# Kernel optimization log

Measured on AMD Instinct MI355X. Metric: run time of the kernel, lower is better.

The kernel has to match this reference:

```python
import jax, jax.numpy as jnp
import numpy as np

N = 50000        # nodes
E = 800000       # edges (avg degree 16)
IN = 256         # in_feature
HID = 32         # hidden per head
HEADS = 4        # gat_heads
OUT = 64         # out_feature
SLOPE = 0.2      # PyG GATConv default negative_slope


def _gat_layer(x, src, dst, edge_weight, W, a_src, a_dst, b, heads, ch, concat):
    """One GATConv: linear -> per-edge attention logits -> segment softmax over
    incoming edges of each dst node -> weighted scatter-sum. edge_weight scales
    the unnormalized attention (log-space edge weighting, identity at init=1)."""
    n = x.shape[0]
    h = (x @ W).reshape(n, heads, ch)                       # [N,H,C]
    al_s = jnp.einsum('nhc,hc->nh', h, a_src)               # [N,H]
    al_d = jnp.einsum('nhc,hc->nh', h, a_dst)               # [N,H]
    logit = jax.nn.leaky_relu(al_s[src] + al_d[dst], SLOPE) # [E,H]
    m = jax.lax.stop_gradient(jax.ops.segment_max(logit, dst, num_segments=n))
    e = jnp.exp(logit - m[dst]) * edge_weight[:, None]      # [E,H]
    denom = jax.ops.segment_sum(e, dst, num_segments=n)     # [N,H]
    alpha = e / (denom[dst] + 1e-16)                        # [E,H]
    out = jax.ops.segment_sum(h[src] * alpha[..., None], dst, num_segments=n)
    out = out.reshape(n, heads * ch) if concat else out.mean(axis=1)
    return out + b


def setup_inputs() -> dict:
    key = jax.random.key(0)
    ks = jax.random.split(key, 14)
    s = 0.1
    x = jax.random.normal(ks[0], (N, IN), jnp.float32)
    edge_index = jax.random.randint(ks[1], (2, E), 0, N, dtype=jnp.int64)
    edge_weight = jnp.ones((E,), jnp.float32)
    D1 = HEADS * HID
    W1 = jax.random.normal(ks[2], (IN, D1), jnp.float32) * s
    a_src1 = jax.random.normal(ks[3], (HEADS, HID), jnp.float32) * s
    a_dst1 = jax.random.normal(ks[4], (HEADS, HID), jnp.float32) * s
    b1 = jnp.zeros((D1,), jnp.float32)
    W2 = jax.random.normal(ks[5], (D1, D1), jnp.float32) * s
    a_src2 = jax.random.normal(ks[6], (HEADS, HID), jnp.float32) * s
    a_dst2 = jax.random.normal(ks[7], (HEADS, HID), jnp.float32) * s
    b2 = jnp.zeros((D1,), jnp.float32)
    W3 = jax.random.normal(ks[8], (D1, OUT), jnp.float32) * s
    a_src3 = jax.random.normal(ks[9], (1, OUT), jnp.float32) * s
    a_dst3 = jax.random.normal(ks[10], (1, OUT), jnp.float32) * s
    b3 = jnp.zeros((OUT,), jnp.float32)
    return dict(x=x, edge_index=edge_index, edge_weight=edge_weight,
                W1=W1, a_src1=a_src1, a_dst1=a_dst1, b1=b1,
                W2=W2, a_src2=a_src2, a_dst2=a_dst2, b2=b2,
                W3=W3, a_src3=a_src3, a_dst3=a_dst3, b3=b3)


def reference(x, edge_index, edge_weight,
              W1, a_src1, a_dst1, b1,
              W2, a_src2, a_dst2, b2,
              W3, a_src3, a_dst3, b3):
    src, dst = edge_index[0], edge_index[1]
    h = _gat_layer(x, src, dst, edge_weight, W1, a_src1, a_dst1, b1, HEADS, HID, True)
    h = jax.nn.relu(h)  # dropout = identity in eval mode
    h = _gat_layer(h, src, dst, edge_weight, W2, a_src2, a_dst2, b2, HEADS, HID, True)
    h = jax.nn.relu(h)
    out = _gat_layer(h, src, dst, edge_weight, W3, a_src3, a_dst3, b3, 1, OUT, False)
    return out
```

## Files before the change

### kernel.cpp

```cpp
#include <hip/hip_runtime.h>
#include <math.h>

#define NNODES 50000
#define NEDGES 800000

#define BIN_SHIFT 9
#define BIN_W 512
#define NBINS 98
#define CAP 12288
#define ATILE 4096
#define NBINBLK ((NEDGES + ATILE - 1) / ATILE)

typedef _Float16 f16;
typedef __attribute__((ext_vector_type(2))) _Float16 f16x2;
typedef __attribute__((ext_vector_type(4))) _Float16 f16x4;
typedef __attribute__((ext_vector_type(8))) _Float16 f16x8;
typedef __attribute__((ext_vector_type(4))) float f32x4;

__device__ __forceinline__ float leaky02(float v) { return v > 0.f ? v : 0.2f * v; }

__device__ __forceinline__ void wave_lds_fence() {
  __asm__ volatile("s_waitcnt lgkmcnt(0)" ::: "memory");
}


__global__ __launch_bounds__(256) void init_kernel(int* __restrict__ binCursor,
                                                   const float* __restrict__ W1,
                                                   const float* __restrict__ W2,
                                                   const float* __restrict__ W3,
                                                   f16* __restrict__ WT1,
                                                   f16* __restrict__ WT2,
                                                   f16* __restrict__ WT3) {
  int gid = blockIdx.x * 256 + threadIdx.x;
  int stride = gridDim.x * 256;
  if (gid < NBINS) binCursor[gid] = 0;
  for (int i = gid; i < 32768; i += stride) {
    int d = i >> 8, k = i & 255;
    WT1[i] = (f16)W1[k * 128 + d];
  }
  for (int i = gid; i < 16384; i += stride) {
    int d = i >> 7, k = i & 127;
    WT2[i] = (f16)W2[k * 128 + d];
  }
  for (int i = gid; i < 8192; i += stride) {
    int d = i >> 7, k = i & 127;
    WT3[i] = (f16)W3[k * 64 + d];
  }
}


__device__ __forceinline__ void bin_body(int bid,
                                         const int* __restrict__ dst,
                                         const int* __restrict__ src,
                                         const float* __restrict__ ew,
                                         int* __restrict__ binCursor,
                                         int2* __restrict__ binned, int ne) {
  __shared__ int cnt[NBINS];
  __shared__ int gbase[NBINS];
  int tid = threadIdx.x;
  int t0 = bid * ATILE;
  if (tid < NBINS) cnt[tid] = 0;
  __syncthreads();
  int saved[ATILE / 256];
  #pragma unroll
  for (int u = 0; u < ATILE / 256; ++u) {
    int i = t0 + u * 256 + tid;
    int v = 0;
    if (i < ne) {
      int d = dst[i];
      int idx = atomicAdd(&cnt[d >> BIN_SHIFT], 1);
      v = d | (idx << 16);
    }
    saved[u] = v;
  }
  __syncthreads();
  if (tid < NBINS) gbase[tid] = atomicAdd(&binCursor[tid], cnt[tid]);
  __syncthreads();
  #pragma unroll
  for (int u = 0; u < ATILE / 256; ++u) {
    int i = t0 + u * 256 + tid;
    if (i < ne) {
      int v = saved[u];
      int d = v & 0xffff;
      int idx = (int)((unsigned)v >> 16);
      int b = d >> BIN_SHIFT;
      int slot = gbase[b] + idx;
      if (slot < CAP)
        binned[(size_t)b * CAP + slot] =
            make_int2(src[i] | (d << 16), __float_as_int(ew[i]));
    }
  }
}


__global__ __launch_bounds__(256) void build_kernel(const int2* __restrict__ binned,
                                                    const int* __restrict__ binCursor,
                                                    int* __restrict__ offsets,
                                                    int2* __restrict__ edgeSW, int n) {
  __shared__ int sizes[NBINS];
  __shared__ int cnt[BIN_W];
  __shared__ int wsum[4];
  __shared__ int bstartS;
  int tid = threadIdx.x;
  int b = blockIdx.x;
  if (tid < NBINS) sizes[tid] = binCursor[tid];
  cnt[tid] = 0;
  cnt[tid + 256] = 0;
  __syncthreads();
  if (tid == 0) {
    int s = 0;
    for (int k = 0; k < b; ++k) s += (sizes[k] < CAP ? sizes[k] : CAP);
    bstartS = s;
  }
  int mySize = sizes[b];
  if (mySize > CAP) mySize = CAP;
  __syncthreads();
  const int2* mybin = binned + (size_t)b * CAP;
  for (int i = tid; i < mySize; i += 256)
    atomicAdd(&cnt[((unsigned)mybin[i].x >> 16) - b * BIN_W], 1);
  __syncthreads();
  int c0 = cnt[2 * tid], c1 = cnt[2 * tid + 1];
  int s2 = c0 + c1;
  int lane = tid & 63, wid = tid >> 6;
  int incl = s2;
  #pragma unroll
  for (int o = 1; o < 64; o <<= 1) {
    int u = __shfl_up(incl, o, 64);
    if (lane >= o) incl += u;
  }
  if (lane == 63) wsum[wid] = incl;
  __syncthreads();
  if (tid == 0) {
    int r = 0;
    #pragma unroll
    for (int w = 0; w < 4; ++w) { int t = wsum[w]; wsum[w] = r; r += t; }
  }
  __syncthreads();
  int excl0 = bstartS + wsum[wid] + incl - s2;
  int excl1 = excl0 + c0;
  int node0 = b * BIN_W;
  if (node0 + 2 * tid < n)     offsets[node0 + 2 * tid]     = excl0;
  if (node0 + 2 * tid + 1 < n) offsets[node0 + 2 * tid + 1] = excl1;
  if (b == NBINS - 1 && tid == 0) offsets[n] = bstartS + mySize;
  __syncthreads();
  cnt[2 * tid] = excl0;
  cnt[2 * tid + 1] = excl1;
  __syncthreads();
  for (int i = tid; i < mySize; i += 256) {
    int2 r = mybin[i];
    int dloc = (int)((unsigned)r.x >> 16) - b * BIN_W;
    int pos = atomicAdd(&cnt[dloc], 1);
    edgeSW[pos] = make_int2(r.x & 0xffff, r.y);
  }
}


template<typename AT, int BN, int H>
__device__ __forceinline__ void gemm_body(int bid,
                                          const AT* __restrict__ A,
                                          const f16* __restrict__ BT,
                                          f16* __restrict__ C,
                                          const float* __restrict__ a_src,
                                          const float* __restrict__ a_dst,
                                          float* __restrict__ als,
                                          float* __restrict__ ald,
                                          int M, int K) {
  constexpr int BM = 64;
  constexpr int WN = BN / 2;
  constexpr int MT = 2, NT = WN / 16;
  __shared__ f16 As[BM * 72];
  __shared__ f16 Bs[BN * 72];
  __shared__ float redS[2][2][32], redD[2][2][32];
  int tid = threadIdx.x;
  int lane = tid & 63, wave = tid >> 6;
  int wm = wave & 1, wn = wave >> 1;
  int row0 = bid * BM;
  int quad = lane >> 4, cc = lane & 15;

  f32x4 acc[MT][NT];
  #pragma unroll
  for (int mt = 0; mt < MT; ++mt)
    #pragma unroll
    for (int nt = 0; nt < NT; ++nt)
      acc[mt][nt] = (f32x4){0.f, 0.f, 0.f, 0.f};

  for (int k0 = 0; k0 < K; k0 += 64) {
    __syncthreads();
    if constexpr (sizeof(AT) == 4) {
      #pragma unroll
      for (int i = 0; i < 4; ++i) {
        int r = i * 16 + (tid >> 4);
        int kc = (tid & 15) * 4;
        float4 av = make_float4(0.f, 0.f, 0.f, 0.f);
        if (row0 + r < M) av = *(const float4*)&A[(size_t)(row0 + r) * K + k0 + kc];
        *(f16x4*)&As[r * 72 + kc] = (f16x4){(f16)av.x, (f16)av.y, (f16)av.z, (f16)av.w};
      }
    } else {
      #pragma unroll
      for (int i = 0; i < 2; ++i) {
        int r = i * 32 + (tid >> 3);
        int kc = (tid & 7) * 8;
        f16x8 hv = {0, 0, 0, 0, 0, 0, 0, 0};
        if (row0 + r < M) hv = *(const f16x8*)&A[(size_t)(row0 + r) * K + k0 + kc];
        *(f16x8*)&As[r * 72 + kc] = hv;
      }
    }
    #pragma unroll
    for (int i = 0; i < BN / 32; ++i) {
      int d = i * 32 + (tid >> 3);
      int kc = (tid & 7) * 8;
      *(f16x8*)&Bs[d * 72 + kc] = *(const f16x8*)&BT[(size_t)d * K + k0 + kc];
    }
    __syncthreads();
    #pragma unroll
    for (int ki = 0; ki < 2; ++ki) {
      f16x8 a[MT], b[NT];
      #pragma unroll
      for (int mt = 0; mt < MT; ++mt)
        a[mt] = *(const f16x8*)&As[(wm * 32 + mt * 16 + cc) * 72 + ki * 32 + quad * 8];
      #pragma unroll
      for (int nt = 0; nt < NT; ++nt)
        b[nt] = *(const f16x8*)&Bs[(wn * WN + nt * 16 + cc) * 72 + ki * 32 + quad * 8];
      #pragma unroll
      for (int mt = 0; mt < MT; ++mt)
        #pragma unroll
        for (int nt = 0; nt < NT; ++nt)
          acc[mt][nt] = __builtin_amdgcn_mfma_f32_16x16x32_f16(a[mt], b[nt], acc[mt][nt], 0, 0, 0);
    }
  }

  float asv[NT], adv[NT];
  #pragma unroll
  for (int nt = 0; nt < NT; ++nt) {
    int ch = wn * WN + nt * 16 + cc;
    asv[nt] = a_src[ch];
    adv[nt] = a_dst[ch];
  }

  #pragma unroll
  for (int mt = 0; mt < MT; ++mt)
    #pragma unroll
    for (int v = 0; v < 4; ++v) {
      int row = row0 + wm * 32 + mt * 16 + quad * 4 + v;
      if (row < M) {
        #pragma unroll
        for (int nt = 0; nt < NT; ++nt)
          C[(size_t)row * BN + wn * WN + nt * 16 + cc] = (f16)acc[mt][nt][v];
      }
      if constexpr (H == 4) {
        float s0 = acc[mt][0][v] * asv[0] + acc[mt][1][v] * asv[1];
        float s1 = acc[mt][2][v] * asv[2] + acc[mt][3][v] * asv[3];
        float d0 = acc[mt][0][v] * adv[0] + acc[mt][1][v] * adv[1];
        float d1 = acc[mt][2][v] * adv[2] + acc[mt][3][v] * adv[3];
        #pragma unroll
        for (int o = 1; o < 16; o <<= 1) {
          s0 += __shfl_xor(s0, o);
          s1 += __shfl_xor(s1, o);
          d0 += __shfl_xor(d0, o);
          d1 += __shfl_xor(d1, o);
        }
        if (cc == 0 && row < M) {
          *(float2*)&als[row * 4 + 2 * wn] = make_float2(s0, s1);
          *(float2*)&ald[row * 4 + 2 * wn] = make_float2(d0, d1);
        }
      } else {
        float s0 = acc[mt][0][v] * asv[0] + acc[mt][1][v] * asv[1];
        float d0 = acc[mt][0][v] * adv[0] + acc[mt][1][v] * adv[1];
        #pragma unroll
        for (int o = 1; o < 16; o <<= 1) {
          s0 += __shfl_xor(s0, o);
          d0 += __shfl_xor(d0, o);
        }
        int r = mt * 16 + quad * 4 + v;
        if (cc == 0) { redS[wm][wn][r] = s0; redD[wm][wn][r] = d0; }
      }
    }
  if constexpr (H == 1) {
    __syncthreads();
    #pragma unroll
    for (int mt = 0; mt < MT; ++mt)
      #pragma unroll
      for (int v = 0; v < 4; ++v) {
        int row = row0 + wm * 32 + mt * 16 + quad * 4 + v;
        int r = mt * 16 + quad * 4 + v;
        if (wn == 0 && cc == 0 && row < M) {
          als[row] = redS[wm][0][r] + redS[wm][1][r];
          ald[row] = redD[wm][0][r] + redD[wm][1][r];
        }
      }
  }
}

template<typename AT, int BN, int H>
__global__ __launch_bounds__(256) void gemm_mfma_kernel(const AT* __restrict__ A,
                                                        const f16* __restrict__ BT,
                                                        f16* __restrict__ C,
                                                        const float* __restrict__ a_src,
                                                        const float* __restrict__ a_dst,
                                                        float* __restrict__ als,
                                                        float* __restrict__ ald,
                                                        int M, int K) {
  gemm_body<AT, BN, H>(blockIdx.x, A, BT, C, a_src, a_dst, als, ald, M, K);
}


__global__ __launch_bounds__(256) void fused_front_kernel(const int* __restrict__ dst,
                                                          const int* __restrict__ src,
                                                          const float* __restrict__ ew,
                                                          int* __restrict__ binCursor,
                                                          int2* __restrict__ binned, int ne,
                                                          const float* __restrict__ A,
                                                          const f16* __restrict__ BT,
                                                          f16* __restrict__ C,
                                                          const float* __restrict__ a_src,
                                                          const float* __restrict__ a_dst,
                                                          float* __restrict__ als,
                                                          float* __restrict__ ald,
                                                          int M, int K) {
  if (blockIdx.x < NBINBLK)
    bin_body(blockIdx.x, dst, src, ew, binCursor, binned, ne);
  else
    gemm_body<float, 128, 4>(blockIdx.x - NBINBLK, A, BT, C, a_src, a_dst, als, ald, M, K);
}


template<bool RELU>
__global__ __launch_bounds__(256) void aggregate4_kernel(const f16* __restrict__ h16,
                                                         const float* __restrict__ als,
                                                         const float* __restrict__ ald,
                                                         const int* __restrict__ offsets,
                                                         const int2* __restrict__ edgeSW,
                                                         const float* __restrict__ bias,
                                                         f16* __restrict__ out, int n_nodes) {
  __shared__ int   swS[8][32];
  __shared__ float swW[8][4][36];
  int hw = threadIdx.x >> 5;
  int hl = threadIdx.x & 31;
  int node = blockIdx.x * 8 + hw;
  bool valid = node < n_nodes;
  int nodeC = valid ? node : n_nodes - 1;
  int start = offsets[nodeC], end = offsets[nodeC + 1];
  int deg = valid ? end - start : 0;

  float4 aldv = *(const float4*)&ald[nodeC * 4];

  int s0 = 0; float wgt0 = 0.f;
  float v0 = 0.f, v1 = 0.f, v2 = 0.f, v3 = 0.f;
  float m0 = -INFINITY, m1 = -INFINITY, m2 = -INFINITY, m3 = -INFINITY;
  if (hl < deg) {
    int2 e = edgeSW[start + hl];
    s0 = e.x;
    wgt0 = __int_as_float(e.y);
    float4 a4 = *(const float4*)&als[s0 * 4];
    v0 = leaky02(a4.x + aldv.x); m0 = v0;
    v1 = leaky02(a4.y + aldv.y); m1 = v1;
    v2 = leaky02(a4.z + aldv.z); m2 = v2;
    v3 = leaky02(a4.w + aldv.w); m3 = v3;
  }
  for (int j = start + 32 + hl; j < end; j += 32) {
    int2 e = edgeSW[j];
    float4 a4 = *(const float4*)&als[e.x * 4];
    m0 = fmaxf(m0, leaky02(a4.x + aldv.x));
    m1 = fmaxf(m1, leaky02(a4.y + aldv.y));
    m2 = fmaxf(m2, leaky02(a4.z + aldv.z));
    m3 = fmaxf(m3, leaky02(a4.w + aldv.w));
  }
  #pragma unroll
  for (int o = 16; o > 0; o >>= 1) {
    m0 = fmaxf(m0, __shfl_xor(m0, o, 32));
    m1 = fmaxf(m1, __shfl_xor(m1, o, 32));
    m2 = fmaxf(m2, __shfl_xor(m2, o, 32));
    m3 = fmaxf(m3, __shfl_xor(m3, o, 32));
  }
  float w0 = 0.f, w1 = 0.f, w2 = 0.f, w3 = 0.f;
  if (hl < deg) {
    w0 = __expf(v0 - m0) * wgt0;
    w1 = __expf(v1 - m1) * wgt0;
    w2 = __expf(v2 - m2) * wgt0;
    w3 = __expf(v3 - m3) * wgt0;
  }
  swS[hw][hl] = s0;
  swW[hw][0][hl] = w0;
  swW[hw][1][hl] = w1;
  swW[hw][2][hl] = w2;
  swW[hw][3][hl] = w3;
  wave_lds_fence();

  int h2 = hl >> 4, l16 = hl & 15;
  int head = l16 >> 2;
  float acc0 = 0.f, acc1 = 0.f, acc2 = 0.f, acc3 = 0.f;
  float acc4 = 0.f, acc5 = 0.f, acc6 = 0.f, acc7 = 0.f;
  float dd = 0.f;
  int cn = deg < 32 ? deg : 32;
  int nb = (cn + 15) >> 4;
  for (int b = 0; b < nb; ++b) {
    int j0 = b * 16 + h2 * 8;
    int4   sa = *(const int4*)&swS[hw][j0];
    int4   sb = *(const int4*)&swS[hw][j0 + 4];
    float4 wa = *(const float4*)&swW[hw][head][j0];
    float4 wb = *(const float4*)&swW[hw][head][j0 + 4];
    int   sj[8] = {sa.x, sa.y, sa.z, sa.w, sb.x, sb.y, sb.z, sb.w};
    float wj[8] = {wa.x, wa.y, wa.z, wa.w, wb.x, wb.y, wb.z, wb.w};
    f16x8 hv[8];
    #pragma unroll
    for (int u = 0; u < 8; ++u)
      hv[u] = *(const f16x8*)&h16[(size_t)sj[u] * 128 + 8 * l16];
    #pragma unroll
    for (int u = 0; u < 8; ++u) {
      dd += wj[u];
      acc0 += wj[u] * (float)hv[u][0];
      acc1 += wj[u] * (float)hv[u][1];
      acc2 += wj[u] * (float)hv[u][2];
      acc3 += wj[u] * (float)hv[u][3];
      acc4 += wj[u] * (float)hv[u][4];
      acc5 += wj[u] * (float)hv[u][5];
      acc6 += wj[u] * (float)hv[u][6];
      acc7 += wj[u] * (float)hv[u][7];
    }
  }
  for (int base = start + 32; base < end; base += 32) {
    int cnt = end - base; if (cnt > 32) cnt = 32;
    int st = 0; float u0 = 0.f, u1 = 0.f, u2 = 0.f, u3 = 0.f;
    if (hl < cnt) {
      int2 e = edgeSW[base + hl];
      st = e.x;
      float wg = __int_as_float(e.y);
      float4 a4 = *(const float4*)&als[st * 4];
      u0 = __expf(leaky02(a4.x + aldv.x) - m0) * wg;
      u1 = __expf(leaky02(a4.y + aldv.y) - m1) * wg;
      u2 = __expf(leaky02(a4.z + aldv.z) - m2) * wg;
      u3 = __expf(leaky02(a4.w + aldv.w) - m3) * wg;
    }
    for (int jj = h2; jj < cnt; jj += 2) {
      int sjr = __shfl(st, jj, 32);
      float t0 = __shfl(u0, jj, 32), t1 = __shfl(u1, jj, 32);
      float t2 = __shfl(u2, jj, 32), t3 = __shfl(u3, jj, 32);
      float wr = head == 0 ? t0 : head == 1 ? t1 : head == 2 ? t2 : t3;
      f16x8 hv = *(const f16x8*)&h16[(size_t)sjr * 128 + 8 * l16];
      dd += wr;
      acc0 += wr * (float)hv[0];
      acc1 += wr * (float)hv[1];
      acc2 += wr * (float)hv[2];
      acc3 += wr * (float)hv[3];
      acc4 += wr * (float)hv[4];
      acc5 += wr * (float)hv[5];
      acc6 += wr * (float)hv[6];
      acc7 += wr * (float)hv[7];
    }
  }

  acc0 += __shfl_xor(acc0, 16, 32);
  acc1 += __shfl_xor(acc1, 16, 32);
  acc2 += __shfl_xor(acc2, 16, 32);
  acc3 += __shfl_xor(acc3, 16, 32);
  acc4 += __shfl_xor(acc4, 16, 32);
  acc5 += __shfl_xor(acc5, 16, 32);
  acc6 += __shfl_xor(acc6, 16, 32);
  acc7 += __shfl_xor(acc7, 16, 32);
  dd   += __shfl_xor(dd, 16, 32);

  if (valid && h2 == 0) {
    float inv = 1.f / (dd + 1e-16f);
    float4 bv0 = *(const float4*)&bias[8 * l16];
    float4 bv1 = *(const float4*)&bias[8 * l16 + 4];
    float o0 = acc0 * inv + bv0.x, o1 = acc1 * inv + bv0.y;
    float o2 = acc2 * inv + bv0.z, o3 = acc3 * inv + bv0.w;
    float o4 = acc4 * inv + bv1.x, o5 = acc5 * inv + bv1.y;
    float o6 = acc6 * inv + bv1.z, o7 = acc7 * inv + bv1.w;
    if (RELU) {
      o0 = fmaxf(o0, 0.f); o1 = fmaxf(o1, 0.f);
      o2 = fmaxf(o2, 0.f); o3 = fmaxf(o3, 0.f);
      o4 = fmaxf(o4, 0.f); o5 = fmaxf(o5, 0.f);
      o6 = fmaxf(o6, 0.f); o7 = fmaxf(o7, 0.f);
    }
    *(f16x8*)&out[(size_t)node * 128 + 8 * l16] =
        (f16x8){(f16)o0, (f16)o1, (f16)o2, (f16)o3, (f16)o4, (f16)o5, (f16)o6, (f16)o7};
  }
}

__global__ __launch_bounds__(256) void aggregate1_kernel(const f16* __restrict__ h16,
                                                         const float* __restrict__ als,
                                                         const float* __restrict__ ald,
                                                         const int* __restrict__ offsets,
                                                         const int2* __restrict__ edgeSW,
                                                         const float* __restrict__ bias,
                                                         float* __restrict__ out, int n_nodes) {
  __shared__ int   s1s[8][32];
  __shared__ float w1s[8][32];
  int hw = threadIdx.x >> 5;
  int hl = threadIdx.x & 31;
  int node = blockIdx.x * 8 + hw;
  bool valid = node < n_nodes;
  int nodeC = valid ? node : n_nodes - 1;
  int start = offsets[nodeC], end = offsets[nodeC + 1];
  int deg = valid ? end - start : 0;

  float ald0 = ald[nodeC];
  int s0 = 0; float wgt0 = 0.f, v0 = 0.f, m0 = -INFINITY;
  if (hl < deg) {
    int2 e = edgeSW[start + hl];
    s0 = e.x;
    wgt0 = __int_as_float(e.y);
    v0 = leaky02(als[s0] + ald0);
    m0 = v0;
  }
  for (int j = start + 32 + hl; j < end; j += 32) {
    int2 e = edgeSW[j];
    m0 = fmaxf(m0, leaky02(als[e.x] + ald0));
  }
  #pragma unroll
  for (int o = 16; o > 0; o >>= 1) m0 = fmaxf(m0, __shfl_xor(m0, o, 32));

  float w0 = (hl < deg) ? __expf(v0 - m0) * wgt0 : 0.f;
  s1s[hw][hl] = s0;
  w1s[hw][hl] = w0;
  wave_lds_fence();

  int h2 = hl >> 4, l16 = hl & 15;
  float aX = 0.f, aY = 0.f, aZ = 0.f, aW = 0.f, dd = 0.f;
  int cn = deg < 32 ? deg : 32;
  int nb = (cn + 15) >> 4;
  for (int b = 0; b < nb; ++b) {
    int j0 = b * 16 + h2 * 8;
    int4   sa = *(const int4*)&s1s[hw][j0];
    int4   sb = *(const int4*)&s1s[hw][j0 + 4];
    float4 wa = *(const float4*)&w1s[hw][j0];
    float4 wb = *(const float4*)&w1s[hw][j0 + 4];
    int   sj[8] = {sa.x, sa.y, sa.z, sa.w, sb.x, sb.y, sb.z, sb.w};
    float wj[8] = {wa.x, wa.y, wa.z, wa.w, wb.x, wb.y, wb.z, wb.w};
    f16x4 hv[8];
    #pragma unroll
    for (int u = 0; u < 8; ++u)
      hv[u] = *(const f16x4*)&h16[(size_t)sj[u] * 64 + 4 * l16];
    #pragma unroll
    for (int u = 0; u < 8; ++u) {
      dd += wj[u];
      aX += wj[u] * (float)hv[u][0];
      aY += wj[u] * (float)hv[u][1];
      aZ += wj[u] * (float)hv[u][2];
      aW += wj[u] * (float)hv[u][3];
    }
  }
  for (int base = start + 32; base < end; base += 32) {
    int cnt = end - base; if (cnt > 32) cnt = 32;
    int st = 0; float u0 = 0.f;
    if (hl < cnt) {
      int2 e = edgeSW[base + hl];
      st = e.x;
      u0 = __expf(leaky02(als[st] + ald0) - m0) * __int_as_float(e.y);
    }
    for (int jj = h2; jj < cnt; jj += 2) {
      int sjr = __shfl(st, jj, 32);
      float wr = __shfl(u0, jj, 32);
      f16x4 hv = *(const f16x4*)&h16[(size_t)sjr * 64 + 4 * l16];
      dd += wr;
      aX += wr * (float)hv[0];
      aY += wr * (float)hv[1];
      aZ += wr * (float)hv[2];
      aW += wr * (float)hv[3];
    }
  }

  aX += __shfl_xor(aX, 16, 32);
  aY += __shfl_xor(aY, 16, 32);
  aZ += __shfl_xor(aZ, 16, 32);
  aW += __shfl_xor(aW, 16, 32);
  dd += __shfl_xor(dd, 16, 32);

  if (valid && h2 == 0) {
    float inv = 1.f / (dd + 1e-16f);
    float4 bv = *(const float4*)&bias[4 * l16];
    float4 ov = make_float4(aX * inv + bv.x, aY * inv + bv.y,
                            aZ * inv + bv.z, aW * inv + bv.w);
    *(float4*)&out[(size_t)node * 64 + 4 * l16] = ov;
  }
}


extern "C" void kernel_launch(void* const* d_in, const int* in_sizes, int n_in,
                              void* d_out, int out_size, void* d_ws, size_t ws_size,
                              hipStream_t stream) {
  const int N = NNODES, E = NEDGES;
  const float* x   = (const float*)d_in[0];
  const int*   ei  = (const int*)d_in[1];
  const float* ew  = (const float*)d_in[2];
  const float* W1  = (const float*)d_in[3];
  const float* as1 = (const float*)d_in[4];
  const float* ad1 = (const float*)d_in[5];
  const float* b1  = (const float*)d_in[6];
  const float* W2  = (const float*)d_in[7];
  const float* as2 = (const float*)d_in[8];
  const float* ad2 = (const float*)d_in[9];
  const float* b2  = (const float*)d_in[10];
  const float* W3  = (const float*)d_in[11];
  const float* as3 = (const float*)d_in[12];
  const float* ad3 = (const float*)d_in[13];
  const float* b3  = (const float*)d_in[14];
  const int* src = ei;
  const int* dst = ei + E;

  uint8_t* p = (uint8_t*)d_ws;
  auto carve = [&](size_t bytes) {
    void* r = (void*)p;
    p += (bytes + 255) & ~(size_t)255;
    return r;
  };
  int*   binCursor = (int*)carve((size_t)NBINS * 4);
  int*   offsets   = (int*)carve((size_t)(N + 1) * 4);
  int2*  binned    = (int2*)carve((size_t)NBINS * CAP * 8);
  int2*  edgeSW    = (int2*)carve((size_t)E * 8);
  float* als1      = (float*)carve((size_t)N * 4 * 4);
  float* ald1      = (float*)carve((size_t)N * 4 * 4);
  float* als2      = (float*)carve((size_t)N * 4 * 4);
  float* ald2      = (float*)carve((size_t)N * 4 * 4);
  float* als3      = (float*)carve((size_t)N * 4);
  float* ald3      = (float*)carve((size_t)N * 4);
  f16*   hA16      = (f16*)carve((size_t)N * 128 * 2);
  f16*   hB16      = (f16*)carve((size_t)N * 128 * 2);
  f16*   hC16      = (f16*)carve((size_t)N * 64 * 2);
  f16*   WT1       = (f16*)carve((size_t)256 * 128 * 2);
  f16*   WT2       = (f16*)carve((size_t)128 * 128 * 2);
  f16*   WT3       = (f16*)carve((size_t)128 * 64 * 2);

  int gemmGrid = (N + 63) / 64;
  int aggGrid = (N + 7) / 8;

  init_kernel<<<128, 256, 0, stream>>>(binCursor, W1, W2, W3, WT1, WT2, WT3);

  fused_front_kernel<<<NBINBLK + gemmGrid, 256, 0, stream>>>(
      dst, src, ew, binCursor, binned, E,
      x, WT1, hA16, as1, ad1, als1, ald1, N, 256);
  build_kernel<<<NBINS, 256, 0, stream>>>(binned, binCursor, offsets, edgeSW, N);

  aggregate4_kernel<true><<<aggGrid, 256, 0, stream>>>(hA16, als1, ald1, offsets, edgeSW,
                                                       b1, hB16, N);
  gemm_mfma_kernel<f16, 128, 4><<<gemmGrid, 256, 0, stream>>>(hB16, WT2, hA16, as2, ad2,
                                                              als2, ald2, N, 128);
  aggregate4_kernel<true><<<aggGrid, 256, 0, stream>>>(hA16, als2, ald2, offsets, edgeSW,
                                                       b2, hB16, N);
  gemm_mfma_kernel<f16, 64, 1><<<gemmGrid, 256, 0, stream>>>(hB16, WT3, hC16, as3, ad3,
                                                             als3, ald3, N, 128);
  aggregate1_kernel<<<aggGrid, 256, 0, stream>>>(hC16, als3, ald3, offsets, edgeSW,
                                                 b3, (float*)d_out, N);
}
```

Measured before the change: 270.8 us.

## Fuse layer aggregation with next-layer GEMM via shared-memory A tile

Layer-1 and layer-2 aggregation are merged with the following GEMM into one 512-thread kernel. Each block aggregates 64 nodes, writes the ReLU'd fp16 features straight into an LDS A-tile, then runs MFMA against the next weight matrix and computes the attention logits. This removes two kernel launches and the global write and re-read of the intermediate hidden features. In exchange, LDS use per block grows and the gather phase and the GEMM phase are serialized inside each block, which may lower occupancy and overlap.

```diff
diff --git a/kernel.cpp b/kernel.cpp
--- a/kernel.cpp
+++ b/kernel.cpp
@@ -170,7 +170,6 @@
   constexpr int MT = 2, NT = WN / 16;
   __shared__ f16 As[BM * 72];
   __shared__ f16 Bs[BN * 72];
-  __shared__ float redS[2][2][32], redD[2][2][32];
   int tid = threadIdx.x;
   int lane = tid & 63, wave = tid >> 6;
   int wm = wave & 1, wn = wave >> 1;
@@ -247,60 +246,22 @@
         for (int nt = 0; nt < NT; ++nt)
           C[(size_t)row * BN + wn * WN + nt * 16 + cc] = (f16)acc[mt][nt][v];
       }
-      if constexpr (H == 4) {
-        float s0 = acc[mt][0][v] * asv[0] + acc[mt][1][v] * asv[1];
-        float s1 = acc[mt][2][v] * asv[2] + acc[mt][3][v] * asv[3];
-        float d0 = acc[mt][0][v] * adv[0] + acc[mt][1][v] * adv[1];
-        float d1 = acc[mt][2][v] * adv[2] + acc[mt][3][v] * adv[3];
-        #pragma unroll
-        for (int o = 1; o < 16; o <<= 1) {
-          s0 += __shfl_xor(s0, o);
-          s1 += __shfl_xor(s1, o);
-          d0 += __shfl_xor(d0, o);
-          d1 += __shfl_xor(d1, o);
-        }
-        if (cc == 0 && row < M) {
-          *(float2*)&als[row * 4 + 2 * wn] = make_float2(s0, s1);
-          *(float2*)&ald[row * 4 + 2 * wn] = make_float2(d0, d1);
-        }
-      } else {
-        float s0 = acc[mt][0][v] * asv[0] + acc[mt][1][v] * asv[1];
-        float d0 = acc[mt][0][v] * adv[0] + acc[mt][1][v] * adv[1];
-        #pragma unroll
-        for (int o = 1; o < 16; o <<= 1) {
-          s0 += __shfl_xor(s0, o);
-          d0 += __shfl_xor(d0, o);
-        }
-        int r = mt * 16 + quad * 4 + v;
-        if (cc == 0) { redS[wm][wn][r] = s0; redD[wm][wn][r] = d0; }
-      }
-    }
-  if constexpr (H == 1) {
-    __syncthreads();
-    #pragma unroll
-    for (int mt = 0; mt < MT; ++mt)
-      #pragma unroll
-      for (int v = 0; v < 4; ++v) {
-        int row = row0 + wm * 32 + mt * 16 + quad * 4 + v;
-        int r = mt * 16 + quad * 4 + v;
-        if (wn == 0 && cc == 0 && row < M) {
-          als[row] = redS[wm][0][r] + redS[wm][1][r];
-          ald[row] = redD[wm][0][r] + redD[wm][1][r];
-        }
-      }
-  }
-}
-
-template<typename AT, int BN, int H>
-__global__ __launch_bounds__(256) void gemm_mfma_kernel(const AT* __restrict__ A,
-                                                        const f16* __restrict__ BT,
-                                                        f16* __restrict__ C,
-                                                        const float* __restrict__ a_src,
-                                                        const float* __restrict__ a_dst,
-                                                        float* __restrict__ als,
-                                                        float* __restrict__ ald,
-                                                        int M, int K) {
-  gemm_body<AT, BN, H>(blockIdx.x, A, BT, C, a_src, a_dst, als, ald, M, K);
+      float s0 = acc[mt][0][v] * asv[0] + acc[mt][1][v] * asv[1];
+      float s1 = acc[mt][2][v] * asv[2] + acc[mt][3][v] * asv[3];
+      float d0 = acc[mt][0][v] * adv[0] + acc[mt][1][v] * adv[1];
+      float d1 = acc[mt][2][v] * adv[2] + acc[mt][3][v] * adv[3];
+      #pragma unroll
+      for (int o = 1; o < 16; o <<= 1) {
+        s0 += __shfl_xor(s0, o);
+        s1 += __shfl_xor(s1, o);
+        d0 += __shfl_xor(d0, o);
+        d1 += __shfl_xor(d1, o);
+      }
+      if (cc == 0 && row < M) {
+        *(float2*)&als[row * 4 + 2 * wn] = make_float2(s0, s1);
+        *(float2*)&ald[row * 4 + 2 * wn] = make_float2(d0, d1);
+      }
+    }
 }
 
 
@@ -324,157 +285,267 @@
 }
 
 
-template<bool RELU>
-__global__ __launch_bounds__(256) void aggregate4_kernel(const f16* __restrict__ h16,
-                                                         const float* __restrict__ als,
-                                                         const float* __restrict__ ald,
-                                                         const int* __restrict__ offsets,
-                                                         const int2* __restrict__ edgeSW,
-                                                         const float* __restrict__ bias,
-                                                         f16* __restrict__ out, int n_nodes) {
-  __shared__ int   swS[8][32];
-  __shared__ float swW[8][4][36];
-  int hw = threadIdx.x >> 5;
-  int hl = threadIdx.x & 31;
-  int node = blockIdx.x * 8 + hw;
-  bool valid = node < n_nodes;
-  int nodeC = valid ? node : n_nodes - 1;
-  int start = offsets[nodeC], end = offsets[nodeC + 1];
-  int deg = valid ? end - start : 0;
-
-  float4 aldv = *(const float4*)&ald[nodeC * 4];
-
-  int s0 = 0; float wgt0 = 0.f;
-  float v0 = 0.f, v1 = 0.f, v2 = 0.f, v3 = 0.f;
-  float m0 = -INFINITY, m1 = -INFINITY, m2 = -INFINITY, m3 = -INFINITY;
-  if (hl < deg) {
-    int2 e = edgeSW[start + hl];
-    s0 = e.x;
-    wgt0 = __int_as_float(e.y);
-    float4 a4 = *(const float4*)&als[s0 * 4];
-    v0 = leaky02(a4.x + aldv.x); m0 = v0;
-    v1 = leaky02(a4.y + aldv.y); m1 = v1;
-    v2 = leaky02(a4.z + aldv.z); m2 = v2;
-    v3 = leaky02(a4.w + aldv.w); m3 = v3;
-  }
-  for (int j = start + 32 + hl; j < end; j += 32) {
-    int2 e = edgeSW[j];
-    float4 a4 = *(const float4*)&als[e.x * 4];
-    m0 = fmaxf(m0, leaky02(a4.x + aldv.x));
-    m1 = fmaxf(m1, leaky02(a4.y + aldv.y));
-    m2 = fmaxf(m2, leaky02(a4.z + aldv.z));
-    m3 = fmaxf(m3, leaky02(a4.w + aldv.w));
-  }
-  #pragma unroll
-  for (int o = 16; o > 0; o >>= 1) {
-    m0 = fmaxf(m0, __shfl_xor(m0, o, 32));
-    m1 = fmaxf(m1, __shfl_xor(m1, o, 32));
-    m2 = fmaxf(m2, __shfl_xor(m2, o, 32));
-    m3 = fmaxf(m3, __shfl_xor(m3, o, 32));
-  }
-  float w0 = 0.f, w1 = 0.f, w2 = 0.f, w3 = 0.f;
-  if (hl < deg) {
-    w0 = __expf(v0 - m0) * wgt0;
-    w1 = __expf(v1 - m1) * wgt0;
-    w2 = __expf(v2 - m2) * wgt0;
-    w3 = __expf(v3 - m3) * wgt0;
-  }
-  swS[hw][hl] = s0;
-  swW[hw][0][hl] = w0;
-  swW[hw][1][hl] = w1;
-  swW[hw][2][hl] = w2;
-  swW[hw][3][hl] = w3;
-  wave_lds_fence();
-
+template<int BN, int H>
+__global__ __launch_bounds__(512) void fused_aggemm_kernel(
+    const f16* __restrict__ hg,
+    const float* __restrict__ als_i,
+    const float* __restrict__ ald_i,
+    const int* __restrict__ offsets,
+    const int2* __restrict__ edgeSW,
+    const float* __restrict__ bias,
+    const f16* __restrict__ BT,
+    f16* __restrict__ C,
+    const float* __restrict__ a_src,
+    const float* __restrict__ a_dst,
+    float* __restrict__ als_o,
+    float* __restrict__ ald_o,
+    int n_nodes) {
+  constexpr int K = 128;
+  constexpr int BM = 64;
+  constexpr int WN = BN / 4;
+  constexpr int MT = 2, NT = WN / 16;
+  __shared__ f16 As[BM * 136];
+  __shared__ f16 Bs[BN * 72];
+  __shared__ int   swS[16][32];
+  __shared__ float swW[16][4][36];
+  __shared__ float redS[2][4][32], redD[2][4][32];
+
+  int tid = threadIdx.x;
+  int hw = tid >> 5, hl = tid & 31;
+  int row0 = blockIdx.x * BM;
   int h2 = hl >> 4, l16 = hl & 15;
   int head = l16 >> 2;
-  float acc0 = 0.f, acc1 = 0.f, acc2 = 0.f, acc3 = 0.f;
-  float acc4 = 0.f, acc5 = 0.f, acc6 = 0.f, acc7 = 0.f;
-  float dd = 0.f;
-  int cn = deg < 32 ? deg : 32;
-  int nb = (cn + 15) >> 4;
-  for (int b = 0; b < nb; ++b) {
-    int j0 = b * 16 + h2 * 8;
-    int4   sa = *(const int4*)&swS[hw][j0];
-    int4   sb = *(const int4*)&swS[hw][j0 + 4];
-    float4 wa = *(const float4*)&swW[hw][head][j0];
-    float4 wb = *(const float4*)&swW[hw][head][j0 + 4];
-    int   sj[8] = {sa.x, sa.y, sa.z, sa.w, sb.x, sb.y, sb.z, sb.w};
-    float wj[8] = {wa.x, wa.y, wa.z, wa.w, wb.x, wb.y, wb.z, wb.w};
-    f16x8 hv[8];
-    #pragma unroll
-    for (int u = 0; u < 8; ++u)
-      hv[u] = *(const f16x8*)&h16[(size_t)sj[u] * 128 + 8 * l16];
-    #pragma unroll
-    for (int u = 0; u < 8; ++u) {
-      dd += wj[u];
-      acc0 += wj[u] * (float)hv[u][0];
-      acc1 += wj[u] * (float)hv[u][1];
-      acc2 += wj[u] * (float)hv[u][2];
-      acc3 += wj[u] * (float)hv[u][3];
-      acc4 += wj[u] * (float)hv[u][4];
-      acc5 += wj[u] * (float)hv[u][5];
-      acc6 += wj[u] * (float)hv[u][6];
-      acc7 += wj[u] * (float)hv[u][7];
-    }
-  }
-  for (int base = start + 32; base < end; base += 32) {
-    int cnt = end - base; if (cnt > 32) cnt = 32;
-    int st = 0; float u0 = 0.f, u1 = 0.f, u2 = 0.f, u3 = 0.f;
-    if (hl < cnt) {
-      int2 e = edgeSW[base + hl];
-      st = e.x;
-      float wg = __int_as_float(e.y);
-      float4 a4 = *(const float4*)&als[st * 4];
-      u0 = __expf(leaky02(a4.x + aldv.x) - m0) * wg;
-      u1 = __expf(leaky02(a4.y + aldv.y) - m1) * wg;
-      u2 = __expf(leaky02(a4.z + aldv.z) - m2) * wg;
-      u3 = __expf(leaky02(a4.w + aldv.w) - m3) * wg;
-    }
-    for (int jj = h2; jj < cnt; jj += 2) {
-      int sjr = __shfl(st, jj, 32);
-      float t0 = __shfl(u0, jj, 32), t1 = __shfl(u1, jj, 32);
-      float t2 = __shfl(u2, jj, 32), t3 = __shfl(u3, jj, 32);
-      float wr = head == 0 ? t0 : head == 1 ? t1 : head == 2 ? t2 : t3;
-      f16x8 hv = *(const f16x8*)&h16[(size_t)sjr * 128 + 8 * l16];
-      dd += wr;
-      acc0 += wr * (float)hv[0];
-      acc1 += wr * (float)hv[1];
-      acc2 += wr * (float)hv[2];
-      acc3 += wr * (float)hv[3];
-      acc4 += wr * (float)hv[4];
-      acc5 += wr * (float)hv[5];
-      acc6 += wr * (float)hv[6];
-      acc7 += wr * (float)hv[7];
-    }
-  }
-
-  acc0 += __shfl_xor(acc0, 16, 32);
-  acc1 += __shfl_xor(acc1, 16, 32);
-  acc2 += __shfl_xor(acc2, 16, 32);
-  acc3 += __shfl_xor(acc3, 16, 32);
-  acc4 += __shfl_xor(acc4, 16, 32);
-  acc5 += __shfl_xor(acc5, 16, 32);
-  acc6 += __shfl_xor(acc6, 16, 32);
-  acc7 += __shfl_xor(acc7, 16, 32);
-  dd   += __shfl_xor(dd, 16, 32);
-
-  if (valid && h2 == 0) {
-    float inv = 1.f / (dd + 1e-16f);
-    float4 bv0 = *(const float4*)&bias[8 * l16];
-    float4 bv1 = *(const float4*)&bias[8 * l16 + 4];
-    float o0 = acc0 * inv + bv0.x, o1 = acc1 * inv + bv0.y;
-    float o2 = acc2 * inv + bv0.z, o3 = acc3 * inv + bv0.w;
-    float o4 = acc4 * inv + bv1.x, o5 = acc5 * inv + bv1.y;
-    float o6 = acc6 * inv + bv1.z, o7 = acc7 * inv + bv1.w;
-    if (RELU) {
-      o0 = fmaxf(o0, 0.f); o1 = fmaxf(o1, 0.f);
-      o2 = fmaxf(o2, 0.f); o3 = fmaxf(o3, 0.f);
-      o4 = fmaxf(o4, 0.f); o5 = fmaxf(o5, 0.f);
-      o6 = fmaxf(o6, 0.f); o7 = fmaxf(o7, 0.f);
-    }
-    *(f16x8*)&out[(size_t)node * 128 + 8 * l16] =
-        (f16x8){(f16)o0, (f16)o1, (f16)o2, (f16)o3, (f16)o4, (f16)o5, (f16)o6, (f16)o7};
+
+  for (int p = 0; p < 4; ++p) {
+    int node = row0 + p * 16 + hw;
+    bool valid = node < n_nodes;
+    int nodeC = valid ? node : n_nodes - 1;
+    int start = offsets[nodeC], end = offsets[nodeC + 1];
+    int deg = valid ? end - start : 0;
+
+    float4 aldv = *(const float4*)&ald_i[nodeC * 4];
+
+    int s0 = 0; float wgt0 = 0.f;
+    float v0 = 0.f, v1 = 0.f, v2 = 0.f, v3 = 0.f;
+    float m0 = -INFINITY, m1 = -INFINITY, m2 = -INFINITY, m3 = -INFINITY;
+    if (hl < deg) {
+      int2 e = edgeSW[start + hl];
+      s0 = e.x;
+      wgt0 = __int_as_float(e.y);
+      float4 a4 = *(const float4*)&als_i[s0 * 4];
+      v0 = leaky02(a4.x + aldv.x); m0 = v0;
+      v1 = leaky02(a4.y + aldv.y); m1 = v1;
+      v2 = leaky02(a4.z + aldv.z); m2 = v2;
+      v3 = leaky02(a4.w + aldv.w); m3 = v3;
+    }
+    for (int j = start + 32 + hl; j < end; j += 32) {
+      int2 e = edgeSW[j];
+      float4 a4 = *(const float4*)&als_i[e.x * 4];
+      m0 = fmaxf(m0, leaky02(a4.x + aldv.x));
+      m1 = fmaxf(m1, leaky02(a4.y + aldv.y));
+      m2 = fmaxf(m2, leaky02(a4.z + aldv.z));
+      m3 = fmaxf(m3, leaky02(a4.w + aldv.w));
+    }
+    #pragma unroll
+    for (int o = 16; o > 0; o >>= 1) {
+      m0 = fmaxf(m0, __shfl_xor(m0, o, 32));
+      m1 = fmaxf(m1, __shfl_xor(m1, o, 32));
+      m2 = fmaxf(m2, __shfl_xor(m2, o, 32));
+      m3 = fmaxf(m3, __shfl_xor(m3, o, 32));
+    }
+    float w0 = 0.f, w1 = 0.f, w2 = 0.f, w3 = 0.f;
+    if (hl < deg) {
+      w0 = __expf(v0 - m0) * wgt0;
+      w1 = __expf(v1 - m1) * wgt0;
+      w2 = __expf(v2 - m2) * wgt0;
+      w3 = __expf(v3 - m3) * wgt0;
+    }
+    swS[hw][hl] = s0;
+    swW[hw][0][hl] = w0;
+    swW[hw][1][hl] = w1;
+    swW[hw][2][hl] = w2;
+    swW[hw][3][hl] = w3;
+    wave_lds_fence();
+
+    float acc0 = 0.f, acc1 = 0.f, acc2 = 0.f, acc3 = 0.f;
+    float acc4 = 0.f, acc5 = 0.f, acc6 = 0.f, acc7 = 0.f;
+    float dd = 0.f;
+    int cn = deg < 32 ? deg : 32;
+    int nb = (cn + 15) >> 4;
+    for (int b = 0; b < nb; ++b) {
+      int j0 = b * 16 + h2 * 8;
+      int4   sa = *(const int4*)&swS[hw][j0];
+      int4   sb = *(const int4*)&swS[hw][j0 + 4];
+      float4 wa = *(const float4*)&swW[hw][head][j0];
+      float4 wb = *(const float4*)&swW[hw][head][j0 + 4];
+      int   sj[8] = {sa.x, sa.y, sa.z, sa.w, sb.x, sb.y, sb.z, sb.w};
+      float wj[8] = {wa.x, wa.y, wa.z, wa.w, wb.x, wb.y, wb.z, wb.w};
+      f16x8 hv[8];
+      #pragma unroll
+      for (int u = 0; u < 8; ++u)
+        hv[u] = *(const f16x8*)&hg[(size_t)sj[u] * 128 + 8 * l16];
+      #pragma unroll
+      for (int u = 0; u < 8; ++u) {
+        dd += wj[u];
+        acc0 += wj[u] * (float)hv[u][0];
+        acc1 += wj[u] * (float)hv[u][1];
+        acc2 += wj[u] * (float)hv[u][2];
+        acc3 += wj[u] * (float)hv[u][3];
+        acc4 += wj[u] * (float)hv[u][4];
+        acc5 += wj[u] * (float)hv[u][5];
+        acc6 += wj[u] * (float)hv[u][6];
+        acc7 += wj[u] * (float)hv[u][7];
+      }
+    }
+    for (int base = start + 32; base < end; base += 32) {
+      int cnt = end - base; if (cnt > 32) cnt = 32;
+      int st = 0; float u0 = 0.f, u1 = 0.f, u2 = 0.f, u3 = 0.f;
+      if (hl < cnt) {
+        int2 e = edgeSW[base + hl];
+        st = e.x;
+        float wg = __int_as_float(e.y);
+        float4 a4 = *(const float4*)&als_i[st * 4];
+        u0 = __expf(leaky02(a4.x + aldv.x) - m0) * wg;
+        u1 = __expf(leaky02(a4.y + aldv.y) - m1) * wg;
+        u2 = __expf(leaky02(a4.z + aldv.z) - m2) * wg;
+        u3 = __expf(leaky02(a4.w + aldv.w) - m3) * wg;
+      }
+      for (int jj = h2; jj < cnt; jj += 2) {
+        int sjr = __shfl(st, jj, 32);
+        float t0 = __shfl(u0, jj, 32), t1 = __shfl(u1, jj, 32);
+        float t2 = __shfl(u2, jj, 32), t3 = __shfl(u3, jj, 32);
+        float wr = head == 0 ? t0 : head == 1 ? t1 : head == 2 ? t2 : t3;
+        f16x8 hv = *(const f16x8*)&hg[(size_t)sjr * 128 + 8 * l16];
+        dd += wr;
+        acc0 += wr * (float)hv[0];
+        acc1 += wr * (float)hv[1];
+        acc2 += wr * (float)hv[2];
+        acc3 += wr * (float)hv[3];
+        acc4 += wr * (float)hv[4];
+        acc5 += wr * (float)hv[5];
+        acc6 += wr * (float)hv[6];
+        acc7 += wr * (float)hv[7];
+      }
+    }
+
+    acc0 += __shfl_xor(acc0, 16, 32);
+    acc1 += __shfl_xor(acc1, 16, 32);
+    acc2 += __shfl_xor(acc2, 16, 32);
+    acc3 += __shfl_xor(acc3, 16, 32);
+    acc4 += __shfl_xor(acc4, 16, 32);
+    acc5 += __shfl_xor(acc5, 16, 32);
+    acc6 += __shfl_xor(acc6, 16, 32);
+    acc7 += __shfl_xor(acc7, 16, 32);
+    dd   += __shfl_xor(dd, 16, 32);
+
+    if (h2 == 0) {
+      f16x8 val = {0, 0, 0, 0, 0, 0, 0, 0};
+      if (valid) {
+        float inv = 1.f / (dd + 1e-16f);
+        float4 bv0 = *(const float4*)&bias[8 * l16];
+        float4 bv1 = *(const float4*)&bias[8 * l16 + 4];
+        float o0 = fmaxf(acc0 * inv + bv0.x, 0.f), o1 = fmaxf(acc1 * inv + bv0.y, 0.f);
+        float o2 = fmaxf(acc2 * inv + bv0.z, 0.f), o3 = fmaxf(acc3 * inv + bv0.w, 0.f);
+        float o4 = fmaxf(acc4 * inv + bv1.x, 0.f), o5 = fmaxf(acc5 * inv + bv1.y, 0.f);
+        float o6 = fmaxf(acc6 * inv + bv1.z, 0.f), o7 = fmaxf(acc7 * inv + bv1.w, 0.f);
+        val = (f16x8){(f16)o0, (f16)o1, (f16)o2, (f16)o3, (f16)o4, (f16)o5, (f16)o6, (f16)o7};
+      }
+      *(f16x8*)&As[(p * 16 + hw) * 136 + 8 * l16] = val;
+    }
+  }
+
+  int lane = tid & 63, wave = tid >> 6;
+  int wm = wave & 1, wn = wave >> 1;
+  int quad = lane >> 4, cc = lane & 15;
+
+  f32x4 acc[MT][NT];
+  #pragma unroll
+  for (int mt = 0; mt < MT; ++mt)
+    #pragma unroll
+    for (int nt = 0; nt < NT; ++nt)
+      acc[mt][nt] = (f32x4){0.f, 0.f, 0.f, 0.f};
+
+  for (int k0 = 0; k0 < K; k0 += 64) {
+    __syncthreads();
+    #pragma unroll
+    for (int i = 0; i < (BN * 8) / 512; ++i) {
+      int idx = i * 512 + tid;
+      int d = idx >> 3, kc = (idx & 7) * 8;
+      *(f16x8*)&Bs[d * 72 + kc] = *(const f16x8*)&BT[(size_t)d * K + k0 + kc];
+    }
+    __syncthreads();
+    #pragma unroll
+    for (int ki = 0; ki < 2; ++ki) {
+      f16x8 a[MT], b[NT];
+      #pragma unroll
+      for (int mt = 0; mt < MT; ++mt)
+        a[mt] = *(const f16x8*)&As[(wm * 32 + mt * 16 + cc) * 136 + k0 + ki * 32 + quad * 8];
+      #pragma unroll
+      for (int nt = 0; nt < NT; ++nt)
+        b[nt] = *(const f16x8*)&Bs[(wn * WN + nt * 16 + cc) * 72 + ki * 32 + quad * 8];
+      #pragma unroll
+      for (int mt = 0; mt < MT; ++mt)
+        #pragma unroll
+        for (int nt = 0; nt < NT; ++nt)
+          acc[mt][nt] = __builtin_amdgcn_mfma_f32_16x16x32_f16(a[mt], b[nt], acc[mt][nt], 0, 0, 0);
+    }
+  }
+
+  float asv[NT], adv[NT];
+  #pragma unroll
+  for (int nt = 0; nt < NT; ++nt) {
+    int ch = wn * WN + nt * 16 + cc;
+    asv[nt] = a_src[ch];
+    adv[nt] = a_dst[ch];
+  }
+
+  #pragma unroll
+  for (int mt = 0; mt < MT; ++mt)
+    #pragma unroll
+    for (int v = 0; v < 4; ++v) {
+      int row = row0 + wm * 32 + mt * 16 + quad * 4 + v;
+      if (row < n_nodes) {
+        #pragma unroll
+        for (int nt = 0; nt < NT; ++nt)
+          C[(size_t)row * BN + wn * WN + nt * 16 + cc] = (f16)acc[mt][nt][v];
+      }
+      if constexpr (H == 4) {
+        float s0 = acc[mt][0][v] * asv[0] + acc[mt][1][v] * asv[1];
+        float d0 = acc[mt][0][v] * adv[0] + acc[mt][1][v] * adv[1];
+        #pragma unroll
+        for (int o = 1; o < 16; o <<= 1) {
+          s0 += __shfl_xor(s0, o);
+          d0 += __shfl_xor(d0, o);
+        }
+        if (cc == 0 && row < n_nodes) {
+          als_o[row * 4 + wn] = s0;
+          ald_o[row * 4 + wn] = d0;
+        }
+      } else {
+        float s0 = acc[mt][0][v] * asv[0];
+        float d0 = acc[mt][0][v] * adv[0];
+        #pragma unroll
+        for (int o = 1; o < 16; o <<= 1) {
+          s0 += __shfl_xor(s0, o);
+          d0 += __shfl_xor(d0, o);
+        }
+        int r = mt * 16 + quad * 4 + v;
+        if (cc == 0) { redS[wm][wn][r] = s0; redD[wm][wn][r] = d0; }
+      }
+    }
+  if constexpr (H == 1) {
+    __syncthreads();
+    #pragma unroll
+    for (int mt = 0; mt < MT; ++mt)
+      #pragma unroll
+      for (int v = 0; v < 4; ++v) {
+        int row = row0 + wm * 32 + mt * 16 + quad * 4 + v;
+        int r = mt * 16 + quad * 4 + v;
+        if (wn == 0 && cc == 0 && row < n_nodes) {
+          als_o[row] = redS[wm][0][r] + redS[wm][1][r] + redS[wm][2][r] + redS[wm][3][r];
+          ald_o[row] = redD[wm][0][r] + redD[wm][1][r] + redD[wm][2][r] + redD[wm][3][r];
+        }
+      }
   }
 }
 
@@ -632,14 +703,12 @@
       x, WT1, hA16, as1, ad1, als1, ald1, N, 256);
   build_kernel<<<NBINS, 256, 0, stream>>>(binned, binCursor, offsets, edgeSW, N);
 
-  aggregate4_kernel<true><<<aggGrid, 256, 0, stream>>>(hA16, als1, ald1, offsets, edgeSW,
-                                                       b1, hB16, N);
-  gemm_mfma_kernel<f16, 128, 4><<<gemmGrid, 256, 0, stream>>>(hB16, WT2, hA16, as2, ad2,
-                                                              als2, ald2, N, 128);
-  aggregate4_kernel<true><<<aggGrid, 256, 0, stream>>>(hA16, als2, ald2, offsets, edgeSW,
-                                                       b2, hB16, N);
-  gemm_mfma_kernel<f16, 64, 1><<<gemmGrid, 256, 0, stream>>>(hB16, WT3, hC16, as3, ad3,
-                                                             als3, ald3, N, 128);
+  fused_aggemm_kernel<128, 4><<<gemmGrid, 512, 0, stream>>>(
+      hA16, als1, ald1, offsets, edgeSW, b1,
+      WT2, hB16, as2, ad2, als2, ald2, N);
+  fused_aggemm_kernel<64, 1><<<gemmGrid, 512, 0, stream>>>(
+      hB16, als2, ald2, offsets, edgeSW, b2,
+      WT3, hC16, as3, ad3, als3, ald3, N);
   aggregate1_kernel<<<aggGrid, 256, 0, stream>>>(hC16, als3, ald3, offsets, edgeSW,
                                                  b3, (float*)d_out, N);
 }
```

After: 267.8 us. No clear change (-1.1%).
